# Performance work log

Hardware: AMD Instinct MI355X
Metric: run time of the kernel (lower is better)

The kernel has to match this reference:

```python
import jax, jax.numpy as jnp
import numpy as np
from jax import lax

N, H, BS = 256, 1024, 128
ALPHA, BETA, SIGMA = 60.0, 20.0, 5.0
EPS = 1e-8


def _mlp_w(key, n_in, n_out):
    return jax.random.normal(key, (n_out, n_in), dtype=jnp.float32) / np.sqrt(n_in)


def setup_inputs() -> dict:
    key = jax.random.key(0)
    ks = jax.random.split(key, 8)
    inp = {
        "t": jnp.zeros((), dtype=jnp.float32),
        "x": jax.random.normal(ks[0], (BS, N), dtype=jnp.float32),
        "Wf1": _mlp_w(ks[1], N, H), "bf1": jnp.zeros((H,), jnp.float32),
        "Wf2": _mlp_w(ks[2], H, N), "bf2": jnp.zeros((N,), jnp.float32),
        "Wg1": _mlp_w(ks[3], N, H), "bg1": jnp.zeros((H,), jnp.float32),
        "Wg2": _mlp_w(ks[4], H, N), "bg2": jnp.zeros((N,), jnp.float32),
        "Wk1": _mlp_w(ks[5], N, H), "bk1": jnp.zeros((H,), jnp.float32),
        "Wk2": _mlp_w(ks[6], H, N), "bk2": jnp.zeros((N,), jnp.float32),
    }
    return inp


def reference(t, x, Wf1, bf1, Wf2, bf2, Wg1, bg1, Wg2, bg2, Wk1, bk1, Wk2, bk2):
    def mlp(u, W1, b1, W2, b2):
        return jnp.tanh(u @ W1.T + b1) @ W2.T + b2

    def k_func(u):
        return mlp(u, Wk1, bk1, Wk2, bk2)

    f_out = mlp(x, Wf1, bf1, Wf2, bf2)          # f_model(t, x); t unused
    k_out = k_func(x)
    G_k_out = mlp(x, Wg1, bg1, Wg2, bg2)        # g_fn(x)[0]
    dx_dt = f_out + G_k_out

    # compute_k_jacobian: torch detaches u, so no grad flows to x here.
    # torch layout: J[b, j, i] = d k_i / d u_j  (transpose of jacfwd output)
    x_d = lax.stop_gradient(x)
    J_fwd = jax.vmap(jax.jacfwd(k_func))(x_d)   # [bs, i_out, j_in]
    J_x = jnp.swapaxes(J_fwd, 1, 2)             # [bs, j, i]

    k_norm = jnp.linalg.norm(k_out, axis=1)                      # [bs]
    Jf = jnp.einsum('bji,bi->bj', J_x, f_out)                    # bmm(J, f)
    Jf_norm = jnp.linalg.norm(Jf, axis=1)
    c1 = Jf_norm - ALPHA * k_norm ** (2 * SIGMA - 1)
    JG = jnp.einsum('bji,bi->bj', J_x, G_k_out)                  # bmm(J, G)
    c2 = jnp.sum(k_out * JG, axis=1) - BETA * k_norm ** (2 * SIGMA)

    mask = (c1 > EPS) | (c2 < -EPS)                              # [bs]
    dx_upd = jnp.where(mask[:, None], jnp.zeros_like(dx_dt), dx_dt)
    return (dx_upd + dx_dt) / 2
```

## Files before the change

kernel.cpp:

```cpp
#include <hip/hip_runtime.h>
#include <stdint.h>

#define N_ 256
#define H_ 1024
#define BS_ 128

#define WS_SK    0
#define WS_OACC  131072
#define WS_OPART 229376
#define WS_JPART 1802240
#define WS_XH    2850816
#define WS_XL    2867200
#define WS_W1H   2883584
#define WS_W1L   3276800
#define WS_W2H   3670016
#define WS_W2L   4063232
#define WS_FLOATS 4456448

typedef __attribute__((ext_vector_type(8))) short short8v;
typedef __attribute__((ext_vector_type(4))) float f32x4;

__device__ __forceinline__ ushort bhi(float v) {
    return (ushort)(__float_as_uint(v) >> 16);
}
__device__ __forceinline__ float btrunc(float v) {
    return __uint_as_float(__float_as_uint(v) & 0xFFFF0000u);
}

__global__ __launch_bounds__(256) void kprep(
    const float* __restrict__ x,
    const float* __restrict__ Wf1, const float* __restrict__ Wg1,
    const float* __restrict__ Wk1,
    const float* __restrict__ Wf2, const float* __restrict__ Wg2,
    const float* __restrict__ Wk2,
    ushort* __restrict__ xh, ushort* __restrict__ xl,
    ushort* __restrict__ w1h, ushort* __restrict__ w1l,
    ushort* __restrict__ w2h, ushort* __restrict__ w2l)
{
    const int T = blockIdx.x * 4 + (threadIdx.x >> 6);
    const int l = threadIdx.x & 63;
    const int c16 = l & 15, g = l >> 4;

    const float* src;
    ushort *ph, *pl;
    int dst;
    if (T < 64) {
        const int rt = T >> 3, ks = T & 7;
        src = x + (rt * 16 + c16) * N_ + ks * 32 + g * 8;
        dst = (T * 64 + l) * 8;
        ph = xh; pl = xl;
    } else if (T < 64 + 1536) {
        const int T2 = T - 64;
        const int m = T2 >> 9, rem = T2 & 511;
        const int htg = rem >> 3, ks = rem & 7;
        const float* W1 = (m == 0) ? Wf1 : (m == 1) ? Wg1 : Wk1;
        src = W1 + (htg * 16 + c16) * N_ + ks * 32 + g * 8;
        dst = ((m << 15) + rem * 64 + l) * 8;
        ph = w1h; pl = w1l;
    } else {
        const int T3 = T - 64 - 1536;
        const int m = T3 >> 9, rem = T3 & 511;
        const int it = rem >> 5, hk = rem & 31;
        const float* W2 = (m == 0) ? Wf2 : (m == 1) ? Wg2 : Wk2;
        src = W2 + (it * 16 + c16) * H_ + hk * 32 + g * 8;
        dst = ((m << 15) + rem * 64 + l) * 8;
        ph = w2h; pl = w2l;
    }
    const float4 a = *(const float4*)src;
    const float4 b = *(const float4*)(src + 4);
    const float s[8] = {a.x, a.y, a.z, a.w, b.x, b.y, b.z, b.w};
    union { short8v v; ushort u[8]; } H, L;
    #pragma unroll
    for (int i = 0; i < 8; ++i) {
        H.u[i] = bhi(s[i]);
        L.u[i] = bhi(s[i] - btrunc(s[i]));
    }
    *(short8v*)(ph + dst) = H.v;
    *(short8v*)(pl + dst) = L.v;
}

__global__ __launch_bounds__(256) void k12m(
    const ushort* __restrict__ xh, const ushort* __restrict__ xl,
    const ushort* __restrict__ w1h, const ushort* __restrict__ w1l,
    const ushort* __restrict__ w2h, const ushort* __restrict__ w2l,
    const float* __restrict__ bf1, const float* __restrict__ bg1,
    const float* __restrict__ bk1,
    const float* __restrict__ bf2, const float* __restrict__ bg2,
    const float* __restrict__ bk2,
    float* __restrict__ sk, float* __restrict__ opart)
{
    const int bx  = blockIdx.x;
    const int sid = (bx & 7) * 48 + (bx >> 3);
    const int m   = sid >> 7;
    const int rem = sid & 127;
    const int hs  = rem >> 3;
    const int rt  = rem & 7;
    const int t = threadIdx.x, w = t >> 6, l = t & 63;
    const int col = l & 15, g = l >> 4;
    const int r0 = rt * 16;

    const float* b1 = (m == 0) ? bf1 : (m == 1) ? bg1 : bk1;
    const float* b2 = (m == 0) ? bf2 : (m == 1) ? bg2 : bk2;

    const short8v* XH  = (const short8v*)xh;
    const short8v* XL  = (const short8v*)xl;
    const short8v* W1H = (const short8v*)w1h + m * 32768;
    const short8v* W1L = (const short8v*)w1l + m * 32768;
    const short8v* W2H = (const short8v*)w2h + m * 32768;
    const short8v* W2L = (const short8v*)w2l + m * 32768;

    __shared__ __align__(16) ushort tsh[1024], tsl[1024];

    const int htile = hs * 4 + w;
    f32x4 acc1 = {0.f, 0.f, 0.f, 0.f};
    #pragma unroll
    for (int ks = 0; ks < 8; ++ks) {
        const short8v axh = XH[(rt * 8 + ks) * 64 + l];
        const short8v axl = XL[(rt * 8 + ks) * 64 + l];
        const short8v bh  = W1H[(htile * 8 + ks) * 64 + l];
        const short8v bl  = W1L[(htile * 8 + ks) * 64 + l];
        acc1 = __builtin_amdgcn_mfma_f32_16x16x32_bf16(axl, bh, acc1, 0, 0, 0);
        acc1 = __builtin_amdgcn_mfma_f32_16x16x32_bf16(axh, bl, acc1, 0, 0, 0);
        acc1 = __builtin_amdgcn_mfma_f32_16x16x32_bf16(axh, bh, acc1, 0, 0, 0);
    }
    {
        const int h  = htile * 16 + col;
        const float bv = b1[h];
        const int hl_ = w * 16 + col;
        const int cb = hl_ >> 3, wi = hl_ & 7;
        #pragma unroll
        for (int j = 0; j < 4; ++j) {
            const int row = g * 4 + j;
            const float v = tanhf(acc1[j] + bv);
            if (m == 2) sk[(r0 + row) * H_ + h] = 1.0f - v * v;
            const int cs = cb ^ (row & 7);
            tsh[row * 64 + cs * 8 + wi] = bhi(v);
            tsl[row * 64 + cs * 8 + wi] = bhi(v - btrunc(v));
        }
    }
    __syncthreads();

    f32x4 acc2[4] = {{0.f,0.f,0.f,0.f}, {0.f,0.f,0.f,0.f},
                     {0.f,0.f,0.f,0.f}, {0.f,0.f,0.f,0.f}};
    #pragma unroll
    for (int ks2 = 0; ks2 < 2; ++ks2) {
        const int cs = (ks2 * 4 + g) ^ (col & 7);
        const short8v ath = *(const short8v*)&tsh[col * 64 + cs * 8];
        const short8v atl = *(const short8v*)&tsl[col * 64 + cs * 8];
        const int hk = hs * 2 + ks2;
        #pragma unroll
        for (int n = 0; n < 4; ++n) {
            const int itg = w * 4 + n;
            const short8v bh = W2H[(itg * 32 + hk) * 64 + l];
            const short8v bl = W2L[(itg * 32 + hk) * 64 + l];
            acc2[n] = __builtin_amdgcn_mfma_f32_16x16x32_bf16(atl, bh, acc2[n], 0, 0, 0);
            acc2[n] = __builtin_amdgcn_mfma_f32_16x16x32_bf16(ath, bl, acc2[n], 0, 0, 0);
            acc2[n] = __builtin_amdgcn_mfma_f32_16x16x32_bf16(ath, bh, acc2[n], 0, 0, 0);
        }
    }
    #pragma unroll
    for (int n = 0; n < 4; ++n) {
        const int i = (w * 4 + n) * 16 + col;
        const float bias = (hs == 0) ? b2[i] : 0.0f;
        #pragma unroll
        for (int j = 0; j < 4; ++j) {
            const int row = g * 4 + j;
            opart[((hs * 3 + m) * BS_ + r0 + row) * N_ + i] = acc2[n][j] + bias;
        }
    }
}

__global__ __launch_bounds__(256) void k25_reduce(
    const float* __restrict__ opart, float* __restrict__ oacc)
{
    const int tid = blockIdx.x * 256 + threadIdx.x;
    float s = 0.f;
    #pragma unroll
    for (int ks = 0; ks < 16; ++ks)
        s += opart[ks * (3 * BS_ * N_) + tid];
    oacc[tid] = s;
}

__global__ __launch_bounds__(256) void k3_vj(
    const float* __restrict__ Wk1, const float* __restrict__ Wk2,
    const float* __restrict__ oacc, const float* __restrict__ sk,
    float* __restrict__ jpart)
{
    const int q  = blockIdx.x & 15;
    const int rp = blockIdx.x >> 4;
    const int t  = threadIdx.x;
    const int r0 = rp * 4;
    const int h0 = q * 64;

    __shared__ float fos[4][256], gos[4][256];
    __shared__ float sfv[4][64], sgv[4][64];

    for (int u = t; u < 1024; u += 256) {
        const int r = u >> 8, i = u & 255;
        fos[r][i] = oacc[(r0 + r) * N_ + i];
        gos[r][i] = oacc[(BS_ + r0 + r) * N_ + i];
    }
    __syncthreads();

    {
        const int hl = t & 63;
        const int rl = t >> 6;
        const int h  = h0 + hl;
        const float* w2 = Wk2 + h;
        float vf = 0.f, vg = 0.f;
        #pragma unroll 8
        for (int c = 0; c < 64; ++c) {
            const float4 of = ((const float4*)fos[rl])[c];
            const float4 og = ((const float4*)gos[rl])[c];
            const float w0  = w2[(4 * c + 0) * H_];
            const float w1v = w2[(4 * c + 1) * H_];
            const float w2v = w2[(4 * c + 2) * H_];
            const float w3  = w2[(4 * c + 3) * H_];
            vf += of.x * w0 + of.y * w1v + of.z * w2v + of.w * w3;
            vg += og.x * w0 + og.y * w1v + og.z * w2v + og.w * w3;
        }
        const float s = sk[(r0 + rl) * H_ + h];
        sfv[rl][hl] = s * vf;
        sgv[rl][hl] = s * vg;
    }
    __syncthreads();

    {
        float jf[4] = {0.f, 0.f, 0.f, 0.f};
        float jg[4] = {0.f, 0.f, 0.f, 0.f};
        const float* w1 = Wk1 + h0 * N_ + t;
        #pragma unroll 4
        for (int c = 0; c < 16; ++c) {
            const float w0  = w1[(4 * c + 0) * N_];
            const float wv1 = w1[(4 * c + 1) * N_];
            const float wv2 = w1[(4 * c + 2) * N_];
            const float wv3 = w1[(4 * c + 3) * N_];
            #pragma unroll
            for (int r = 0; r < 4; ++r) {
                const float4 sf = ((const float4*)sfv[r])[c];
                const float4 sg = ((const float4*)sgv[r])[c];
                jf[r] += sf.x * w0 + sf.y * wv1 + sf.z * wv2 + sf.w * wv3;
                jg[r] += sg.x * w0 + sg.y * wv1 + sg.z * wv2 + sg.w * wv3;
            }
        }
        #pragma unroll
        for (int r = 0; r < 4; ++r) {
            jpart[((q * 2 + 0) * BS_ + r0 + r) * N_ + t] = jf[r];
            jpart[((q * 2 + 1) * BS_ + r0 + r) * N_ + t] = jg[r];
        }
    }
}

__global__ __launch_bounds__(256) void k4_final(
    const float* __restrict__ oacc,
    const float* __restrict__ jpart,
    float* __restrict__ out)
{
    const int r = blockIdx.x;
    const int t = threadIdx.x;
    __shared__ float red[12];

    const float fo = oacc[r * N_ + t];
    const float go = oacc[(BS_ + r) * N_ + t];
    const float ko = oacc[(2 * BS_ + r) * N_ + t];

    float jf = 0.f, jg = 0.f;
    #pragma unroll
    for (int q = 0; q < 16; ++q) {
        jf += jpart[((q * 2 + 0) * BS_ + r) * N_ + t];
        jg += jpart[((q * 2 + 1) * BS_ + r) * N_ + t];
    }

    float v0 = ko * ko, v1 = jf * jf, v2 = ko * jg;
    #pragma unroll
    for (int o = 32; o > 0; o >>= 1) {
        v0 += __shfl_xor(v0, o, 64);
        v1 += __shfl_xor(v1, o, 64);
        v2 += __shfl_xor(v2, o, 64);
    }
    const int wid = t >> 6;
    if ((t & 63) == 0) {
        red[wid * 3 + 0] = v0;
        red[wid * 3 + 1] = v1;
        red[wid * 3 + 2] = v2;
    }
    __syncthreads();
    const float kn2 = red[0] + red[3] + red[6] + red[9];
    const float jf2 = red[1] + red[4] + red[7] + red[10];
    const float kjg = red[2] + red[5] + red[8] + red[11];

    const float knorm = sqrtf(kn2);
    const float kn4 = kn2 * kn2;
    const float kn8 = kn4 * kn4;
    const float c1 = sqrtf(jf2) - 60.0f * kn8 * knorm;
    const float c2 = kjg - 20.0f * kn8 * kn2;
    const float scale = ((c1 > 1e-8f) || (c2 < -1e-8f)) ? 0.5f : 1.0f;

    out[r * N_ + t] = (fo + go) * scale;
}

__global__ __launch_bounds__(256) void manifold_fused(
    const float* __restrict__ x,
    const float* __restrict__ Wf1, const float* __restrict__ bf1v,
    const float* __restrict__ Wf2, const float* __restrict__ bf2v,
    const float* __restrict__ Wg1, const float* __restrict__ bg1v,
    const float* __restrict__ Wg2, const float* __restrict__ bg2v,
    const float* __restrict__ Wk1, const float* __restrict__ bk1v,
    const float* __restrict__ Wk2, const float* __restrict__ bk2v,
    float* __restrict__ out)
{
    const int b = blockIdx.x;
    const int t = threadIdx.x;
    __shared__ float xs[N_];
    __shared__ float tf[H_], tg[H_], tk[H_], sk[H_];
    __shared__ float fo[N_], go[N_];
    __shared__ float sfv[H_], sgv[H_];
    __shared__ float red[12];

    xs[t] = x[b * N_ + t];
    __syncthreads();
    {
        float acc[12];
        const float4* rows[12];
        #pragma unroll
        for (int m = 0; m < 4; ++m) {
            const int h = t + m * 256;
            rows[m]     = (const float4*)(Wf1 + h * N_);
            rows[4 + m] = (const float4*)(Wg1 + h * N_);
            rows[8 + m] = (const float4*)(Wk1 + h * N_);
            acc[m] = bf1v[h]; acc[4 + m] = bg1v[h]; acc[8 + m] = bk1v[h];
        }
        const float4* xs4 = (const float4*)xs;
        #pragma unroll 2
        for (int c = 0; c < 64; ++c) {
            float4 a = xs4[c];
            #pragma unroll
            for (int r = 0; r < 12; ++r) {
                float4 w = rows[r][c];
                acc[r] += w.x * a.x + w.y * a.y + w.z * a.z + w.w * a.w;
            }
        }
        #pragma unroll
        for (int m = 0; m < 4; ++m) {
            const int h = t + m * 256;
            float vtf = tanhf(acc[m]);
            float vtg = tanhf(acc[4 + m]);
            float vtk = tanhf(acc[8 + m]);
            tf[h] = vtf; tg[h] = vtg; tk[h] = vtk; sk[h] = 1.0f - vtk * vtk;
        }
    }
    __syncthreads();
    float af = bf2v[t], ag = bg2v[t], ak = bk2v[t];
    {
        const float4* rf = (const float4*)(Wf2 + t * H_);
        const float4* rg = (const float4*)(Wg2 + t * H_);
        const float4* rk = (const float4*)(Wk2 + t * H_);
        #pragma unroll 2
        for (int c = 0; c < 256; ++c) {
            float4 wf = rf[c], wg = rg[c], wk = rk[c];
            float4 vf = ((const float4*)tf)[c];
            af += wf.x*vf.x + wf.y*vf.y + wf.z*vf.z + wf.w*vf.w;
            float4 vg = ((const float4*)tg)[c];
            ag += wg.x*vg.x + wg.y*vg.y + wg.z*vg.z + wg.w*vg.w;
            float4 vk = ((const float4*)tk)[c];
            ak += wk.x*vk.x + wk.y*vk.y + wk.z*vk.z + wk.w*vk.w;
        }
    }
    fo[t] = af; go[t] = ag;
    __syncthreads();
    {
        float vf[4] = {0.f,0.f,0.f,0.f}, vg[4] = {0.f,0.f,0.f,0.f};
        const float* base = Wk2 + 4 * t;
        #pragma unroll 4
        for (int i = 0; i < N_; ++i) {
            float4 w = *(const float4*)(base + i * H_);
            float fv = fo[i], gv = go[i];
            vf[0]+=w.x*fv; vf[1]+=w.y*fv; vf[2]+=w.z*fv; vf[3]+=w.w*fv;
            vg[0]+=w.x*gv; vg[1]+=w.y*gv; vg[2]+=w.z*gv; vg[3]+=w.w*gv;
        }
        #pragma unroll
        for (int c = 0; c < 4; ++c) {
            sfv[4*t+c] = sk[4*t+c]*vf[c];
            sgv[4*t+c] = sk[4*t+c]*vg[c];
        }
    }
    __syncthreads();
    float jf = 0.f, jg = 0.f;
    {
        const float* col = Wk1 + t;
        #pragma unroll 4
        for (int c = 0; c < 256; ++c) {
            float4 s4 = ((const float4*)sfv)[c];
            float4 g4 = ((const float4*)sgv)[c];
            const int h = c * 4;
            float w0 = col[(h+0)*N_], w1 = col[(h+1)*N_];
            float w2 = col[(h+2)*N_], w3 = col[(h+3)*N_];
            jf += s4.x*w0 + s4.y*w1 + s4.z*w2 + s4.w*w3;
            jg += g4.x*w0 + g4.y*w1 + g4.z*w2 + g4.w*w3;
        }
    }
    float v0 = ak*ak, v1 = jf*jf, v2 = ak*jg;
    #pragma unroll
    for (int o = 32; o > 0; o >>= 1) {
        v0 += __shfl_xor(v0, o, 64);
        v1 += __shfl_xor(v1, o, 64);
        v2 += __shfl_xor(v2, o, 64);
    }
    const int wid = t >> 6;
    if ((t & 63) == 0) {
        red[wid*3+0] = v0; red[wid*3+1] = v1; red[wid*3+2] = v2;
    }
    __syncthreads();
    const float kn2 = red[0]+red[3]+red[6]+red[9];
    const float jf2 = red[1]+red[4]+red[7]+red[10];
    const float kjg = red[2]+red[5]+red[8]+red[11];
    const float knorm = sqrtf(kn2);
    const float kn4 = kn2*kn2, kn8 = kn4*kn4;
    const float c1 = sqrtf(jf2) - 60.0f*kn8*knorm;
    const float c2 = kjg - 20.0f*kn8*kn2;
    const float scale = ((c1 > 1e-8f) || (c2 < -1e-8f)) ? 0.5f : 1.0f;
    out[b*N_+t] = (af+ag)*scale;
}

extern "C" void kernel_launch(void* const* d_in, const int* in_sizes, int n_in,
                              void* d_out, int out_size, void* d_ws, size_t ws_size,
                              hipStream_t stream) {
    const float* x    = (const float*)d_in[1];
    const float* Wf1  = (const float*)d_in[2];
    const float* bf1v = (const float*)d_in[3];
    const float* Wf2  = (const float*)d_in[4];
    const float* bf2v = (const float*)d_in[5];
    const float* Wg1  = (const float*)d_in[6];
    const float* bg1v = (const float*)d_in[7];
    const float* Wg2  = (const float*)d_in[8];
    const float* bg2v = (const float*)d_in[9];
    const float* Wk1  = (const float*)d_in[10];
    const float* bk1v = (const float*)d_in[11];
    const float* Wk2  = (const float*)d_in[12];
    const float* bk2v = (const float*)d_in[13];
    float* out = (float*)d_out;

    if (ws_size < (size_t)WS_FLOATS * sizeof(float)) {
        manifold_fused<<<BS_, 256, 0, stream>>>(
            x, Wf1, bf1v, Wf2, bf2v, Wg1, bg1v, Wg2, bg2v,
            Wk1, bk1v, Wk2, bk2v, out);
        return;
    }

    float* ws    = (float*)d_ws;
    float* sk    = ws + WS_SK;
    float* oacc  = ws + WS_OACC;
    float* opart = ws + WS_OPART;
    float* jpart = ws + WS_JPART;
    ushort* xh  = (ushort*)(ws + WS_XH);
    ushort* xl  = (ushort*)(ws + WS_XL);
    ushort* w1h = (ushort*)(ws + WS_W1H);
    ushort* w1l = (ushort*)(ws + WS_W1L);
    ushort* w2h = (ushort*)(ws + WS_W2H);
    ushort* w2l = (ushort*)(ws + WS_W2L);

    kprep     <<<784, 256, 0, stream>>>(x, Wf1, Wg1, Wk1, Wf2, Wg2, Wk2,
                                        xh, xl, w1h, w1l, w2h, w2l);
    k12m      <<<384, 256, 0, stream>>>(xh, xl, w1h, w1l, w2h, w2l,
                                        bf1v, bg1v, bk1v, bf2v, bg2v, bk2v,
                                        sk, opart);
    k25_reduce<<<384, 256, 0, stream>>>(opart, oacc);
    k3_vj     <<<512, 256, 0, stream>>>(Wk1, Wk2, oacc, sk, jpart);
    k4_final  <<<BS_, 256, 0, stream>>>(oacc, jpart, out);
}
```

Before: 114.8 us.

## Fuse bf16 split conversion into GEMM kernel and fold partial reduction into consumers

The separate prep kernel that split x and the weights into hi/lo bf16 arrays is removed. The GEMM kernel now loads fp32 tiles, converts them on the fly and stages them in shared memory before the MFMAs. The standalone reduction kernel is also removed, and the downstream kernels sum the 16 partial outputs themselves. This cuts two launches and the workspace round trips. In exchange each GEMM block redoes conversion work, 384 blocks re-read overlapping weights, and the consumers do redundant partial sums.

```diff
diff --git a/kernel.cpp b/kernel.cpp
--- a/kernel.cpp
+++ b/kernel.cpp
@@ -6,16 +6,9 @@
 #define BS_ 128
 
 #define WS_SK    0
-#define WS_OACC  131072
-#define WS_OPART 229376
-#define WS_JPART 1802240
-#define WS_XH    2850816
-#define WS_XL    2867200
-#define WS_W1H   2883584
-#define WS_W1L   3276800
-#define WS_W2H   3670016
-#define WS_W2L   4063232
-#define WS_FLOATS 4456448
+#define WS_OPART 131072
+#define WS_JPART 1703936
+#define WS_FLOATS 2752512
 
 typedef __attribute__((ext_vector_type(8))) short short8v;
 typedef __attribute__((ext_vector_type(4))) float f32x4;
@@ -27,66 +20,14 @@
     return __uint_as_float(__float_as_uint(v) & 0xFFFF0000u);
 }
 
-__global__ __launch_bounds__(256) void kprep(
+__global__ __launch_bounds__(256) void k12f(
     const float* __restrict__ x,
-    const float* __restrict__ Wf1, const float* __restrict__ Wg1,
-    const float* __restrict__ Wk1,
-    const float* __restrict__ Wf2, const float* __restrict__ Wg2,
-    const float* __restrict__ Wk2,
-    ushort* __restrict__ xh, ushort* __restrict__ xl,
-    ushort* __restrict__ w1h, ushort* __restrict__ w1l,
-    ushort* __restrict__ w2h, ushort* __restrict__ w2l)
-{
-    const int T = blockIdx.x * 4 + (threadIdx.x >> 6);
-    const int l = threadIdx.x & 63;
-    const int c16 = l & 15, g = l >> 4;
-
-    const float* src;
-    ushort *ph, *pl;
-    int dst;
-    if (T < 64) {
-        const int rt = T >> 3, ks = T & 7;
-        src = x + (rt * 16 + c16) * N_ + ks * 32 + g * 8;
-        dst = (T * 64 + l) * 8;
-        ph = xh; pl = xl;
-    } else if (T < 64 + 1536) {
-        const int T2 = T - 64;
-        const int m = T2 >> 9, rem = T2 & 511;
-        const int htg = rem >> 3, ks = rem & 7;
-        const float* W1 = (m == 0) ? Wf1 : (m == 1) ? Wg1 : Wk1;
-        src = W1 + (htg * 16 + c16) * N_ + ks * 32 + g * 8;
-        dst = ((m << 15) + rem * 64 + l) * 8;
-        ph = w1h; pl = w1l;
-    } else {
-        const int T3 = T - 64 - 1536;
-        const int m = T3 >> 9, rem = T3 & 511;
-        const int it = rem >> 5, hk = rem & 31;
-        const float* W2 = (m == 0) ? Wf2 : (m == 1) ? Wg2 : Wk2;
-        src = W2 + (it * 16 + c16) * H_ + hk * 32 + g * 8;
-        dst = ((m << 15) + rem * 64 + l) * 8;
-        ph = w2h; pl = w2l;
-    }
-    const float4 a = *(const float4*)src;
-    const float4 b = *(const float4*)(src + 4);
-    const float s[8] = {a.x, a.y, a.z, a.w, b.x, b.y, b.z, b.w};
-    union { short8v v; ushort u[8]; } H, L;
-    #pragma unroll
-    for (int i = 0; i < 8; ++i) {
-        H.u[i] = bhi(s[i]);
-        L.u[i] = bhi(s[i] - btrunc(s[i]));
-    }
-    *(short8v*)(ph + dst) = H.v;
-    *(short8v*)(pl + dst) = L.v;
-}
-
-__global__ __launch_bounds__(256) void k12m(
-    const ushort* __restrict__ xh, const ushort* __restrict__ xl,
-    const ushort* __restrict__ w1h, const ushort* __restrict__ w1l,
-    const ushort* __restrict__ w2h, const ushort* __restrict__ w2l,
-    const float* __restrict__ bf1, const float* __restrict__ bg1,
-    const float* __restrict__ bk1,
-    const float* __restrict__ bf2, const float* __restrict__ bg2,
-    const float* __restrict__ bk2,
+    const float* __restrict__ Wf1, const float* __restrict__ bf1,
+    const float* __restrict__ Wg1, const float* __restrict__ bg1,
+    const float* __restrict__ Wk1, const float* __restrict__ bk1,
+    const float* __restrict__ Wf2, const float* __restrict__ bf2,
+    const float* __restrict__ Wg2, const float* __restrict__ bg2,
+    const float* __restrict__ Wk2, const float* __restrict__ bk2,
     float* __restrict__ sk, float* __restrict__ opart)
 {
     const int bx  = blockIdx.x;
@@ -99,31 +40,71 @@
     const int col = l & 15, g = l >> 4;
     const int r0 = rt * 16;
 
+    const float* W1 = (m == 0) ? Wf1 : (m == 1) ? Wg1 : Wk1;
     const float* b1 = (m == 0) ? bf1 : (m == 1) ? bg1 : bk1;
+    const float* W2 = (m == 0) ? Wf2 : (m == 1) ? Wg2 : Wk2;
     const float* b2 = (m == 0) ? bf2 : (m == 1) ? bg2 : bk2;
 
-    const short8v* XH  = (const short8v*)xh;
-    const short8v* XL  = (const short8v*)xl;
-    const short8v* W1H = (const short8v*)w1h + m * 32768;
-    const short8v* W1L = (const short8v*)w1l + m * 32768;
-    const short8v* W2H = (const short8v*)w2h + m * 32768;
-    const short8v* W2L = (const short8v*)w2l + m * 32768;
-
+    __shared__ __align__(16) ushort xfh[4096], xfl[4096];
+    __shared__ __align__(16) ushort wfh[8192], wfl[8192];
     __shared__ __align__(16) ushort tsh[1024], tsl[1024];
 
-    const int htile = hs * 4 + w;
+    #pragma unroll
+    for (int p = 0; p < 2; ++p) {
+        const int u  = t + 256 * p;
+        const int ks = u >> 6, ll = u & 63;
+        const float* src = x + (r0 + (ll & 15)) * N_ + ks * 32 + (ll >> 4) * 8;
+        const float4 a = *(const float4*)src;
+        const float4 b = *(const float4*)(src + 4);
+        const float s[8] = {a.x, a.y, a.z, a.w, b.x, b.y, b.z, b.w};
+        union { short8v v; ushort q[8]; } Hh, Ll;
+        #pragma unroll
+        for (int i = 0; i < 8; ++i) {
+            Hh.q[i] = bhi(s[i]);
+            Ll.q[i] = bhi(s[i] - btrunc(s[i]));
+        }
+        *(short8v*)(xfh + u * 8) = Hh.v;
+        *(short8v*)(xfl + u * 8) = Ll.v;
+    }
+
     f32x4 acc1 = {0.f, 0.f, 0.f, 0.f};
     #pragma unroll
-    for (int ks = 0; ks < 8; ++ks) {
-        const short8v axh = XH[(rt * 8 + ks) * 64 + l];
-        const short8v axl = XL[(rt * 8 + ks) * 64 + l];
-        const short8v bh  = W1H[(htile * 8 + ks) * 64 + l];
-        const short8v bl  = W1L[(htile * 8 + ks) * 64 + l];
-        acc1 = __builtin_amdgcn_mfma_f32_16x16x32_bf16(axl, bh, acc1, 0, 0, 0);
-        acc1 = __builtin_amdgcn_mfma_f32_16x16x32_bf16(axh, bl, acc1, 0, 0, 0);
-        acc1 = __builtin_amdgcn_mfma_f32_16x16x32_bf16(axh, bh, acc1, 0, 0, 0);
-    }
-    {
+    for (int kc = 0; kc < 2; ++kc) {
+        #pragma unroll
+        for (int p = 0; p < 4; ++p) {
+            const int u    = t + 256 * p;
+            const int tile = u >> 6, ll = u & 63;
+            const int row  = hs * 64 + (tile >> 2) * 16 + (ll & 15);
+            const int k    = (kc * 4 + (tile & 3)) * 32 + (ll >> 4) * 8;
+            const float* src = W1 + row * N_ + k;
+            const float4 a = *(const float4*)src;
+            const float4 b = *(const float4*)(src + 4);
+            const float s[8] = {a.x, a.y, a.z, a.w, b.x, b.y, b.z, b.w};
+            union { short8v v; ushort q[8]; } Hh, Ll;
+            #pragma unroll
+            for (int i = 0; i < 8; ++i) {
+                Hh.q[i] = bhi(s[i]);
+                Ll.q[i] = bhi(s[i] - btrunc(s[i]));
+            }
+            *(short8v*)(wfh + u * 8) = Hh.v;
+            *(short8v*)(wfl + u * 8) = Ll.v;
+        }
+        __syncthreads();
+        #pragma unroll
+        for (int ksl = 0; ksl < 4; ++ksl) {
+            const short8v axh = *(const short8v*)(xfh + ((kc * 4 + ksl) * 64 + l) * 8);
+            const short8v axl = *(const short8v*)(xfl + ((kc * 4 + ksl) * 64 + l) * 8);
+            const short8v bh  = *(const short8v*)(wfh + ((w * 4 + ksl) * 64 + l) * 8);
+            const short8v bl  = *(const short8v*)(wfl + ((w * 4 + ksl) * 64 + l) * 8);
+            acc1 = __builtin_amdgcn_mfma_f32_16x16x32_bf16(axl, bh, acc1, 0, 0, 0);
+            acc1 = __builtin_amdgcn_mfma_f32_16x16x32_bf16(axh, bl, acc1, 0, 0, 0);
+            acc1 = __builtin_amdgcn_mfma_f32_16x16x32_bf16(axh, bh, acc1, 0, 0, 0);
+        }
+        __syncthreads();
+    }
+
+    {
+        const int htile = hs * 4 + w;
         const int h  = htile * 16 + col;
         const float bv = b1[h];
         const int hl_ = w * 16 + col;
@@ -143,21 +124,41 @@
     f32x4 acc2[4] = {{0.f,0.f,0.f,0.f}, {0.f,0.f,0.f,0.f},
                      {0.f,0.f,0.f,0.f}, {0.f,0.f,0.f,0.f}};
     #pragma unroll
-    for (int ks2 = 0; ks2 < 2; ++ks2) {
-        const int cs = (ks2 * 4 + g) ^ (col & 7);
-        const short8v ath = *(const short8v*)&tsh[col * 64 + cs * 8];
-        const short8v atl = *(const short8v*)&tsl[col * 64 + cs * 8];
-        const int hk = hs * 2 + ks2;
+    for (int hkl = 0; hkl < 2; ++hkl) {
+        #pragma unroll
+        for (int p = 0; p < 4; ++p) {
+            const int u    = t + 256 * p;
+            const int tile = u >> 6, ll = u & 63;
+            const int i    = tile * 16 + (ll & 15);
+            const int kh   = (hs * 2 + hkl) * 32 + (ll >> 4) * 8;
+            const float* src = W2 + i * H_ + kh;
+            const float4 a = *(const float4*)src;
+            const float4 b = *(const float4*)(src + 4);
+            const float s[8] = {a.x, a.y, a.z, a.w, b.x, b.y, b.z, b.w};
+            union { short8v v; ushort q[8]; } Hh, Ll;
+            #pragma unroll
+            for (int i2 = 0; i2 < 8; ++i2) {
+                Hh.q[i2] = bhi(s[i2]);
+                Ll.q[i2] = bhi(s[i2] - btrunc(s[i2]));
+            }
+            *(short8v*)(wfh + u * 8) = Hh.v;
+            *(short8v*)(wfl + u * 8) = Ll.v;
+        }
+        __syncthreads();
+        const int cs = (hkl * 4 + g) ^ (col & 7);
+        const short8v ath = *(const short8v*)(tsh + col * 64 + cs * 8);
+        const short8v atl = *(const short8v*)(tsl + col * 64 + cs * 8);
         #pragma unroll
         for (int n = 0; n < 4; ++n) {
-            const int itg = w * 4 + n;
-            const short8v bh = W2H[(itg * 32 + hk) * 64 + l];
-            const short8v bl = W2L[(itg * 32 + hk) * 64 + l];
+            const short8v bh = *(const short8v*)(wfh + ((w * 4 + n) * 64 + l) * 8);
+            const short8v bl = *(const short8v*)(wfl + ((w * 4 + n) * 64 + l) * 8);
             acc2[n] = __builtin_amdgcn_mfma_f32_16x16x32_bf16(atl, bh, acc2[n], 0, 0, 0);
             acc2[n] = __builtin_amdgcn_mfma_f32_16x16x32_bf16(ath, bl, acc2[n], 0, 0, 0);
             acc2[n] = __builtin_amdgcn_mfma_f32_16x16x32_bf16(ath, bh, acc2[n], 0, 0, 0);
         }
-    }
+        __syncthreads();
+    }
+
     #pragma unroll
     for (int n = 0; n < 4; ++n) {
         const int i = (w * 4 + n) * 16 + col;
@@ -170,20 +171,9 @@
     }
 }
 
-__global__ __launch_bounds__(256) void k25_reduce(
-    const float* __restrict__ opart, float* __restrict__ oacc)
-{
-    const int tid = blockIdx.x * 256 + threadIdx.x;
-    float s = 0.f;
-    #pragma unroll
-    for (int ks = 0; ks < 16; ++ks)
-        s += opart[ks * (3 * BS_ * N_) + tid];
-    oacc[tid] = s;
-}
-
-__global__ __launch_bounds__(256) void k3_vj(
+__global__ __launch_bounds__(256) void k3s(
     const float* __restrict__ Wk1, const float* __restrict__ Wk2,
-    const float* __restrict__ oacc, const float* __restrict__ sk,
+    const float* __restrict__ opart, const float* __restrict__ sk,
     float* __restrict__ jpart)
 {
     const int q  = blockIdx.x & 15;
@@ -197,8 +187,13 @@
 
     for (int u = t; u < 1024; u += 256) {
         const int r = u >> 8, i = u & 255;
-        fos[r][i] = oacc[(r0 + r) * N_ + i];
-        gos[r][i] = oacc[(BS_ + r0 + r) * N_ + i];
+        float sf = 0.f, sg = 0.f;
+        #pragma unroll
+        for (int ks = 0; ks < 16; ++ks) {
+            sf += opart[((ks * 3 + 0) * BS_ + r0 + r) * N_ + i];
+            sg += opart[((ks * 3 + 1) * BS_ + r0 + r) * N_ + i];
+        }
+        fos[r][i] = sf; gos[r][i] = sg;
     }
     __syncthreads();
 
@@ -251,8 +246,8 @@
     }
 }
 
-__global__ __launch_bounds__(256) void k4_final(
-    const float* __restrict__ oacc,
+__global__ __launch_bounds__(256) void k4s(
+    const float* __restrict__ opart,
     const float* __restrict__ jpart,
     float* __restrict__ out)
 {
@@ -260,9 +255,13 @@
     const int t = threadIdx.x;
     __shared__ float red[12];
 
-    const float fo = oacc[r * N_ + t];
-    const float go = oacc[(BS_ + r) * N_ + t];
-    const float ko = oacc[(2 * BS_ + r) * N_ + t];
+    float fo = 0.f, go = 0.f, ko = 0.f;
+    #pragma unroll
+    for (int ks = 0; ks < 16; ++ks) {
+        fo += opart[((ks * 3 + 0) * BS_ + r) * N_ + t];
+        go += opart[((ks * 3 + 1) * BS_ + r) * N_ + t];
+        ko += opart[((ks * 3 + 2) * BS_ + r) * N_ + t];
+    }
 
     float jf = 0.f, jg = 0.f;
     #pragma unroll
@@ -449,22 +448,12 @@
 
     float* ws    = (float*)d_ws;
     float* sk    = ws + WS_SK;
-    float* oacc  = ws + WS_OACC;
     float* opart = ws + WS_OPART;
     float* jpart = ws + WS_JPART;
-    ushort* xh  = (ushort*)(ws + WS_XH);
-    ushort* xl  = (ushort*)(ws + WS_XL);
-    ushort* w1h = (ushort*)(ws + WS_W1H);
-    ushort* w1l = (ushort*)(ws + WS_W1L);
-    ushort* w2h = (ushort*)(ws + WS_W2H);
-    ushort* w2l = (ushort*)(ws + WS_W2L);
-
-    kprep     <<<784, 256, 0, stream>>>(x, Wf1, Wg1, Wk1, Wf2, Wg2, Wk2,
-                                        xh, xl, w1h, w1l, w2h, w2l);
-    k12m      <<<384, 256, 0, stream>>>(xh, xl, w1h, w1l, w2h, w2l,
-                                        bf1v, bg1v, bk1v, bf2v, bg2v, bk2v,
-                                        sk, opart);
-    k25_reduce<<<384, 256, 0, stream>>>(opart, oacc);
-    k3_vj     <<<512, 256, 0, stream>>>(Wk1, Wk2, oacc, sk, jpart);
-    k4_final  <<<BS_, 256, 0, stream>>>(oacc, jpart, out);
-}
+
+    k12f<<<384, 256, 0, stream>>>(x, Wf1, bf1v, Wg1, bg1v, Wk1, bk1v,
+                                  Wf2, bf2v, Wg2, bg2v, Wk2, bk2v,
+                                  sk, opart);
+    k3s <<<512, 256, 0, stream>>>(Wk1, Wk2, opart, sk, jpart);
+    k4s <<<BS_, 256, 0, stream>>>(opart, jpart, out);
+}
```

Measured after the change: 114.9 us. Within noise of the previous version (+0.1%).
